# Performance work log

Hardware: AMD Instinct MI355X
Metric: run time of the kernel (lower is better)

Reference implementation:

```python
import jax, jax.numpy as jnp
import numpy as np

EPS = 1e-08

def _compute_W(V, C, eps=EPS):
    # W = H_k ... H_1, applied sequentially as in the torch loop
    W = jnp.eye(C, dtype=V.dtype)
    def step(W, v):
        v = v / (jnp.linalg.norm(v) + eps)
        # H @ W = W - 2 v (v^T W)
        W = W - 2.0 * jnp.outer(v, v @ W)
        return W, None
    W, _ = jax.lax.scan(step, W, V)
    return W

def setup_inputs() -> dict:
    key = jax.random.key(0)
    k1, k2 = jax.random.split(key)
    x = jax.random.normal(k1, (16, 512, 64, 64), dtype=jnp.float32)
    V = jax.random.normal(k2, (32, 512), dtype=jnp.float32)
    return {"x": x, "V": V}

def reference(x, V):
    B, C, H, Wd = x.shape
    W = _compute_W(V, C)  # [C, C] orthogonal
    # 1x1 conv: out[b,o,h,w] = sum_c W[o,c] * x[b,c,h,w]
    return jnp.einsum('oc,bchw->bohw', W, x)
```

## Files before the change

### kernel.cpp

```cpp
#include <hip/hip_runtime.h>
#include <hip/hip_bf16.h>
#include <stdint.h>
#include <stddef.h>

#define HH_EPS 1e-8f

typedef __attribute__((ext_vector_type(8))) short short8;
typedef __attribute__((ext_vector_type(4))) short short4_t;
typedef __attribute__((ext_vector_type(4))) float f32x4;

#define CDIM 512
#define SDIM 4096
#define BN 128
#define BK 32
#define NSTEP 16

__device__ __forceinline__ size_t wt_idx(int o, int c) {
    return (((size_t)(c >> 5) * 32 + (o >> 4)) * 64
            + (size_t)((c >> 3) & 3) * 16 + (o & 15)) * 8 + (c & 7);
}

__global__ void compute_w(const float* __restrict__ V,
                          __hip_bfloat16* __restrict__ Wt) {
    const int wave = threadIdx.x >> 6;
    const int lane = threadIdx.x & 63;
    const int jA = (blockIdx.x * 4 + wave) * 2;
    const int jB = jA + 1;
    const int ib = lane * 8;

    float wA[8], wB[8];
    #pragma unroll
    for (int r = 0; r < 8; r++) {
        wA[r] = (ib + r == jA) ? 1.0f : 0.0f;
        wB[r] = (ib + r == jB) ? 1.0f : 0.0f;
    }
    float4 c0 = *(const float4*)(V + ib);
    float4 c1 = *(const float4*)(V + ib + 4);

    for (int k = 0; k < 32; k++) {
        const float v[8] = {c0.x, c0.y, c0.z, c0.w, c1.x, c1.y, c1.z, c1.w};
        if (k < 31) {
            c0 = *(const float4*)(V + (size_t)(k + 1) * 512 + ib);
            c1 = *(const float4*)(V + (size_t)(k + 1) * 512 + ib + 4);
        }
        float dA = 0.0f, dB = 0.0f, ss = 0.0f;
        #pragma unroll
        for (int r = 0; r < 8; r++) {
            dA += v[r] * wA[r];
            dB += v[r] * wB[r];
            ss += v[r] * v[r];
        }
        #pragma unroll
        for (int off = 32; off > 0; off >>= 1) {
            dA += __shfl_xor(dA, off);
            dB += __shfl_xor(dB, off);
            ss += __shfl_xor(ss, off);
        }
        const float t = sqrtf(ss) + HH_EPS;
        const float scale = 2.0f / (t * t);
        const float tA = scale * dA, tB = scale * dB;
        #pragma unroll
        for (int r = 0; r < 8; r++) {
            wA[r] -= tA * v[r];
            wB[r] -= tB * v[r];
        }
    }
    #pragma unroll
    for (int r = 0; r < 8; r++) {
        Wt[wt_idx(ib + r, jA)] = __float2bfloat16(wA[r]);
        Wt[wt_idx(ib + r, jB)] = __float2bfloat16(wB[r]);
    }
}

__device__ __forceinline__ void lds_barrier() {
    __builtin_amdgcn_s_waitcnt(0xC07F);
    __builtin_amdgcn_s_barrier();
}

__global__ __launch_bounds__(1024, 4) void hh_gemm(
    const float* __restrict__ x,
    const __hip_bfloat16* __restrict__ Wt,
    float* __restrict__ out)
{
    __shared__ __attribute__((aligned(16))) __hip_bfloat16 Bbuf[2][BN * BK];

    const int tid  = threadIdx.x;
    const int wave = tid >> 6, lane = tid & 63;
    const int quad = lane >> 4, l16 = lane & 15;

    const int bid = blockIdx.x;
    const int b   = bid >> 5;
    const int nt  = bid & 31;
    const int n0  = nt * BN;

    const int c_s  = tid & 127;
    const int r0_s = (tid >> 7) * 4;
    const int kq_s = tid >> 8;
    const int h_s  = (tid >> 7) & 1;
    const float* xp0 = x + (size_t)b * CDIM * SDIM
                         + (size_t)r0_s * SDIM + n0 + c_s;

    const short8* wp = (const short8*)Wt + (size_t)(wave * 2) * 64 + lane;

    f32x4 acc[8][2];
    #pragma unroll
    for (int mi = 0; mi < 8; mi++)
        #pragma unroll
        for (int oi = 0; oi < 2; oi++) {
            f32x4 z = {0.0f, 0.0f, 0.0f, 0.0f};
            acc[mi][oi] = z;
        }

    float  pfB[2][4];
    short8 wb[2][2];

    auto loadB = [&](int kt, int s) {
        const float* p = xp0 + (size_t)kt * BK * SDIM;
        #pragma unroll
        for (int j = 0; j < 4; j++) pfB[s][j] = p[(size_t)j * SDIM];
    };
    auto writeB = [&](int buf, int s) {
        short4_t pk;
        #pragma unroll
        for (int j = 0; j < 4; j++) {
            __hip_bfloat16 h = __float2bfloat16(pfB[s][j]);
            pk[j] = *(const short*)&h;
        }
        *(short4_t*)(&Bbuf[buf][(size_t)(c_s >> 4) * 512
                                + (size_t)(kq_s * 16 + (c_s & 15)) * 8
                                + h_s * 4]) = pk;
    };
    auto loadW = [&](int kt, int s) {
        const short8* p = wp + (size_t)kt * 32 * 64;
        wb[s][0] = p[0];
        wb[s][1] = p[64];
    };

    loadB(0, 0);
    loadB(1, 1);
    loadW(0, 0);
    writeB(0, 0);
    lds_barrier();

    #pragma unroll
    for (int kt = 0; kt < NSTEP; kt++) {
        const int p = kt & 1, w = kt & 1;
        if (kt + 1 < NSTEP) loadW(kt + 1, w ^ 1);
        if (kt + 2 < NSTEP) loadB(kt + 2, kt & 1);
        #pragma unroll
        for (int mi = 0; mi < 8; mi++) {
            const short8 afr =
                *(const short8*)(&Bbuf[p][(size_t)(mi * 64 + lane) * 8]);
            #pragma unroll
            for (int oi = 0; oi < 2; oi++)
                acc[mi][oi] = __builtin_amdgcn_mfma_f32_16x16x32_bf16(
                    afr, wb[w][oi], acc[mi][oi], 0, 0, 0);
        }
        if (kt + 1 < NSTEP) {
            writeB(p ^ 1, (kt + 1) & 1);
            lds_barrier();
        }
    }

    float* ob = out + (size_t)b * CDIM * SDIM + n0;
    #pragma unroll
    for (int oi = 0; oi < 2; oi++) {
        const int o = wave * 32 + oi * 16 + l16;
        #pragma unroll
        for (int mi = 0; mi < 8; mi++)
            *(f32x4*)(ob + (size_t)o * SDIM + mi * 16 + quad * 4) = acc[mi][oi];
    }
}

extern "C" void kernel_launch(void* const* d_in, const int* in_sizes, int n_in,
                              void* d_out, int out_size, void* d_ws, size_t ws_size,
                              hipStream_t stream) {
    const float* x = (const float*)d_in[0];
    const float* V = (const float*)d_in[1];
    float* out = (float*)d_out;

    __hip_bfloat16* Wt = (__hip_bfloat16*)d_ws;

    compute_w<<<64, 256, 0, stream>>>(V, Wt);
    hh_gemm<<<512, 1024, 0, stream>>>(x, Wt, out);
}
```

Measured before the change: 265.6 us.

## Double K tile to 64 and load W fragments inline without prefetch

Raises the K tile from 32 to 64 channels, which halves the number of pipeline steps and LDS barriers. Each thread now loads 8 rows of x and writes one 16-byte bf16 vector to LDS instead of 8 bytes. The register double-buffer of W fragments is dropped, and W is loaded from global/L2 right before each half-step's MFMAs. This exposes W load latency and doubles the LDS buffer size to 32KB.

```diff
diff --git a/kernel.cpp b/kernel.cpp
--- a/kernel.cpp
+++ b/kernel.cpp
@@ -6,14 +6,13 @@
 #define HH_EPS 1e-8f
 
 typedef __attribute__((ext_vector_type(8))) short short8;
-typedef __attribute__((ext_vector_type(4))) short short4_t;
 typedef __attribute__((ext_vector_type(4))) float f32x4;
 
 #define CDIM 512
 #define SDIM 4096
 #define BN 128
-#define BK 32
-#define NSTEP 16
+#define BK 64
+#define NSTEP 8
 
 __device__ __forceinline__ size_t wt_idx(int o, int c) {
     return (((size_t)(c >> 5) * 32 + (o >> 4)) * 64
@@ -93,12 +92,12 @@
     const int nt  = bid & 31;
     const int n0  = nt * BN;
 
-    const int c_s  = tid & 127;
-    const int r0_s = (tid >> 7) * 4;
-    const int kq_s = tid >> 8;
-    const int h_s  = (tid >> 7) & 1;
+    const int c_s = tid & 127;
+    const int o8  = tid >> 7;
     const float* xp0 = x + (size_t)b * CDIM * SDIM
-                         + (size_t)r0_s * SDIM + n0 + c_s;
+                         + (size_t)(o8 * 8) * SDIM + n0 + c_s;
+    const size_t wslot = ((size_t)((o8 >> 2) * 8 + (c_s >> 4)) * 64
+                          + (size_t)((o8 & 3) * 16 + (c_s & 15))) * 8;
 
     const short8* wp = (const short8*)Wt + (size_t)(wave * 2) * 64 + lane;
 
@@ -111,50 +110,47 @@
             acc[mi][oi] = z;
         }
 
-    float  pfB[2][4];
-    short8 wb[2][2];
+    float pfB[2][8];
 
     auto loadB = [&](int kt, int s) {
         const float* p = xp0 + (size_t)kt * BK * SDIM;
         #pragma unroll
-        for (int j = 0; j < 4; j++) pfB[s][j] = p[(size_t)j * SDIM];
+        for (int j = 0; j < 8; j++) pfB[s][j] = p[(size_t)j * SDIM];
     };
     auto writeB = [&](int buf, int s) {
-        short4_t pk;
+        short8 pk;
         #pragma unroll
-        for (int j = 0; j < 4; j++) {
+        for (int j = 0; j < 8; j++) {
             __hip_bfloat16 h = __float2bfloat16(pfB[s][j]);
             pk[j] = *(const short*)&h;
         }
-        *(short4_t*)(&Bbuf[buf][(size_t)(c_s >> 4) * 512
-                                + (size_t)(kq_s * 16 + (c_s & 15)) * 8
-                                + h_s * 4]) = pk;
-    };
-    auto loadW = [&](int kt, int s) {
-        const short8* p = wp + (size_t)kt * 32 * 64;
-        wb[s][0] = p[0];
-        wb[s][1] = p[64];
+        *(short8*)(&Bbuf[buf][wslot]) = pk;
     };
 
     loadB(0, 0);
     loadB(1, 1);
-    loadW(0, 0);
     writeB(0, 0);
     lds_barrier();
 
     #pragma unroll
     for (int kt = 0; kt < NSTEP; kt++) {
-        const int p = kt & 1, w = kt & 1;
-        if (kt + 1 < NSTEP) loadW(kt + 1, w ^ 1);
+        const int p = kt & 1;
         if (kt + 2 < NSTEP) loadB(kt + 2, kt & 1);
         #pragma unroll
-        for (int mi = 0; mi < 8; mi++) {
-            const short8 afr =
-                *(const short8*)(&Bbuf[p][(size_t)(mi * 64 + lane) * 8]);
+        for (int kk = 0; kk < 2; kk++) {
+            short8 wf[2];
+            const short8* wq = wp + ((size_t)(kt * 2 + kk) * 32) * 64;
+            wf[0] = wq[0];
+            wf[1] = wq[64];
             #pragma unroll
-            for (int oi = 0; oi < 2; oi++)
-                acc[mi][oi] = __builtin_amdgcn_mfma_f32_16x16x32_bf16(
-                    afr, wb[w][oi], acc[mi][oi], 0, 0, 0);
+            for (int mi = 0; mi < 8; mi++) {
+                const short8 afr = *(const short8*)(
+                    &Bbuf[p][(size_t)((kk * 8 + mi) * 64 + lane) * 8]);
+                acc[mi][0] = __builtin_amdgcn_mfma_f32_16x16x32_bf16(
+                    afr, wf[0], acc[mi][0], 0, 0, 0);
+                acc[mi][1] = __builtin_amdgcn_mfma_f32_16x16x32_bf16(
+                    afr, wf[1], acc[mi][1], 0, 0, 0);
+            }
         }
         if (kt + 1 < NSTEP) {
             writeB(p ^ 1, (kt + 1) & 1);
```

Measured after the change: 264.7 us. No clear change (-0.4%).

## Vectorize x loads as float4, transpose via lane shuffles, deepen prefetch, remap blocks

Applied to the files above, without the earlier changes.

Each thread now loads x with a single float4 along the spatial dimension instead of four strided scalar loads down the channel dimension. The bf16 values are transposed into the MFMA operand layout with cross-lane shuffles before the LDS write. The x prefetch is deepened from two to three stages. Block indices are permuted so neighbouring blocks spread across batches, which may change cache and XCD locality. This aims to cut the number of global load instructions and improve coalescing, at the cost of extra shuffle and ALU work per step and more registers.

```diff
diff --git a/kernel.cpp b/kernel.cpp
--- a/kernel.cpp
+++ b/kernel.cpp
@@ -6,8 +6,8 @@
 #define HH_EPS 1e-8f
 
 typedef __attribute__((ext_vector_type(8))) short short8;
-typedef __attribute__((ext_vector_type(4))) short short4_t;
 typedef __attribute__((ext_vector_type(4))) float f32x4;
+typedef __attribute__((ext_vector_type(2))) unsigned int uint2_t;
 
 #define CDIM 512
 #define SDIM 4096
@@ -77,6 +77,11 @@
     __builtin_amdgcn_s_barrier();
 }
 
+__device__ __forceinline__ unsigned int bf16u(float f) {
+    __hip_bfloat16 h = __float2bfloat16(f);
+    return (unsigned int)*(unsigned short*)&h;
+}
+
 __global__ __launch_bounds__(1024, 4) void hh_gemm(
     const float* __restrict__ x,
     const __hip_bfloat16* __restrict__ Wt,
@@ -88,17 +93,21 @@
     const int wave = tid >> 6, lane = tid & 63;
     const int quad = lane >> 4, l16 = lane & 15;
 
-    const int bid = blockIdx.x;
+    const int bid = (blockIdx.x & 7) * 64 + (blockIdx.x >> 3);
     const int b   = bid >> 5;
     const int nt  = bid & 31;
     const int n0  = nt * BN;
 
-    const int c_s  = tid & 127;
-    const int r0_s = (tid >> 7) * 4;
-    const int kq_s = tid >> 8;
-    const int h_s  = (tid >> 7) & 1;
+    const int r_t    = lane >> 4;
+    const int kbase  = (wave & 7) * 4;
+    const int k_loc  = kbase + r_t;
+    const int n_loc  = (wave >> 3) * 64 + l16 * 4;
     const float* xp0 = x + (size_t)b * CDIM * SDIM
-                         + (size_t)r0_s * SDIM + n0 + c_s;
+                         + (size_t)k_loc * SDIM + n0 + n_loc;
+    const int n_tr   = (wave >> 3) * 64 + l16 * 4 + r_t;
+    const size_t wslot = ((size_t)(n_tr >> 4) * 64
+                          + (size_t)((wave & 7) >> 1) * 16 + (n_tr & 15)) * 8
+                         + (size_t)(wave & 1) * 4;
 
     const short8* wp = (const short8*)Wt + (size_t)(wave * 2) * 64 + lane;
 
@@ -111,33 +120,42 @@
             acc[mi][oi] = z;
         }
 
-    float  pfB[2][4];
+    float4 pfX[3];
     short8 wb[2][2];
 
-    auto loadB = [&](int kt, int s) {
-        const float* p = xp0 + (size_t)kt * BK * SDIM;
-        #pragma unroll
-        for (int j = 0; j < 4; j++) pfB[s][j] = p[(size_t)j * SDIM];
-    };
-    auto writeB = [&](int buf, int s) {
-        short4_t pk;
-        #pragma unroll
-        for (int j = 0; j < 4; j++) {
-            __hip_bfloat16 h = __float2bfloat16(pfB[s][j]);
-            pk[j] = *(const short*)&h;
-        }
-        *(short4_t*)(&Bbuf[buf][(size_t)(c_s >> 4) * 512
-                                + (size_t)(kq_s * 16 + (c_s & 15)) * 8
-                                + h_s * 4]) = pk;
+    auto loadX = [&](int kt, int s) {
+        pfX[s] = *(const float4*)(xp0 + (size_t)kt * BK * SDIM);
     };
     auto loadW = [&](int kt, int s) {
         const short8* p = wp + (size_t)kt * 32 * 64;
         wb[s][0] = p[0];
         wb[s][1] = p[64];
     };
-
-    loadB(0, 0);
-    loadB(1, 1);
+    auto writeB = [&](int buf, int s) {
+        const float4 v = pfX[s];
+        unsigned int A = bf16u(v.x) | (bf16u(v.y) << 16);
+        unsigned int B = bf16u(v.z) | (bf16u(v.w) << 16);
+        const unsigned int A1 = __shfl_xor((int)A, 16);
+        const unsigned int B1 = __shfl_xor((int)B, 16);
+        unsigned int pA, pB;
+        if ((r_t & 1) == 0) {
+            pA = (A & 0xffffu) | (A1 << 16);
+            pB = (B & 0xffffu) | (B1 << 16);
+        } else {
+            pA = (A1 >> 16) | (A & 0xffff0000u);
+            pB = (B1 >> 16) | (B & 0xffff0000u);
+        }
+        const unsigned int pA2 = __shfl_xor((int)pA, 32);
+        const unsigned int pB2 = __shfl_xor((int)pB, 32);
+        uint2_t w2;
+        if (r_t < 2) { w2[0] = pA;  w2[1] = pA2; }
+        else         { w2[0] = pB2; w2[1] = pB;  }
+        *(uint2_t*)(&Bbuf[buf][wslot]) = w2;
+    };
+
+    loadX(0, 0);
+    loadX(1, 1);
+    loadX(2, 2);
     loadW(0, 0);
     writeB(0, 0);
     lds_barrier();
@@ -146,18 +164,18 @@
     for (int kt = 0; kt < NSTEP; kt++) {
         const int p = kt & 1, w = kt & 1;
         if (kt + 1 < NSTEP) loadW(kt + 1, w ^ 1);
-        if (kt + 2 < NSTEP) loadB(kt + 2, kt & 1);
+        if (kt + 3 < NSTEP) loadX(kt + 3, kt % 3);
         #pragma unroll
         for (int mi = 0; mi < 8; mi++) {
             const short8 afr =
                 *(const short8*)(&Bbuf[p][(size_t)(mi * 64 + lane) * 8]);
-            #pragma unroll
-            for (int oi = 0; oi < 2; oi++)
-                acc[mi][oi] = __builtin_amdgcn_mfma_f32_16x16x32_bf16(
-                    afr, wb[w][oi], acc[mi][oi], 0, 0, 0);
+            acc[mi][0] = __builtin_amdgcn_mfma_f32_16x16x32_bf16(
+                afr, wb[w][0], acc[mi][0], 0, 0, 0);
+            acc[mi][1] = __builtin_amdgcn_mfma_f32_16x16x32_bf16(
+                afr, wb[w][1], acc[mi][1], 0, 0, 0);
         }
         if (kt + 1 < NSTEP) {
-            writeB(p ^ 1, (kt + 1) & 1);
+            writeB(p ^ 1, (kt + 1) % 3);
             lds_barrier();
         }
     }
```

Result: no change. 266.6 us (+0.4%).

## Split GEMM k-step into four barrier-separated phases interleaving loads with MFMA

Applied to the files above, without the earlier changes.

Each k-step of the bf16 MFMA GEMM is broken into four phases. Each phase issues two LDS fragment reads and one slice of the prefetch work (W load, x load, bf16 pack, LDS write), then runs four MFMAs at raised wave priority, with workgroup barriers around each phase. The aim is a ping-pong style schedule where memory issue and matrix work across the 16 waves stay in lockstep and overlap. The cost is eight barriers per k-step instead of one, which in a 1024-thread block may add stall time, and the waitcnt placement after the barrier may not strictly order the LDS write ahead of readers of the next buffer.

```diff
diff --git a/kernel.cpp b/kernel.cpp
--- a/kernel.cpp
+++ b/kernel.cpp
@@ -99,6 +99,8 @@
     const int h_s  = (tid >> 7) & 1;
     const float* xp0 = x + (size_t)b * CDIM * SDIM
                          + (size_t)r0_s * SDIM + n0 + c_s;
+    const size_t wslot = (size_t)(c_s >> 4) * 512
+                       + (size_t)(kq_s * 16 + (c_s & 15)) * 8 + h_s * 4;
 
     const short8* wp = (const short8*)Wt + (size_t)(wave * 2) * 64 + lane;
 
@@ -111,24 +113,24 @@
             acc[mi][oi] = z;
         }
 
-    float  pfB[2][4];
-    short8 wb[2][2];
+    float    pfB[2][4];
+    short8   wb[2][2];
+    short4_t pk;
 
     auto loadB = [&](int kt, int s) {
         const float* p = xp0 + (size_t)kt * BK * SDIM;
         #pragma unroll
         for (int j = 0; j < 4; j++) pfB[s][j] = p[(size_t)j * SDIM];
     };
-    auto writeB = [&](int buf, int s) {
-        short4_t pk;
+    auto packB = [&](int s) {
         #pragma unroll
         for (int j = 0; j < 4; j++) {
             __hip_bfloat16 h = __float2bfloat16(pfB[s][j]);
             pk[j] = *(const short*)&h;
         }
-        *(short4_t*)(&Bbuf[buf][(size_t)(c_s >> 4) * 512
-                                + (size_t)(kq_s * 16 + (c_s & 15)) * 8
-                                + h_s * 4]) = pk;
+    };
+    auto writePK = [&](int buf) {
+        *(short4_t*)(&Bbuf[buf][wslot]) = pk;
     };
     auto loadW = [&](int kt, int s) {
         const short8* p = wp + (size_t)kt * 32 * 64;
@@ -136,31 +138,55 @@
         wb[s][1] = p[64];
     };
 
+#define MFMA1(A, MI, OI)                                                       \
+    acc[MI][OI] = __builtin_amdgcn_mfma_f32_16x16x32_bf16(                     \
+        A, wb[P_][OI], acc[MI][OI], 0, 0, 0);
+
+#define PHASE(P_, Q, STAGE)                                                    \
+    {                                                                          \
+        const short8 a0 = *(const short8*)(                                    \
+            &Bbuf[P_][(size_t)(((Q) * 2 + 0) * 64 + lane) * 8]);               \
+        const short8 a1 = *(const short8*)(                                    \
+            &Bbuf[P_][(size_t)(((Q) * 2 + 1) * 64 + lane) * 8]);               \
+        STAGE;                                                                 \
+        __builtin_amdgcn_s_barrier();                                          \
+        __builtin_amdgcn_s_waitcnt(0xC07F);      \
+        __builtin_amdgcn_s_setprio(1);                                         \
+        acc[(Q)*2+0][0] = __builtin_amdgcn_mfma_f32_16x16x32_bf16(             \
+            a0, wb[P_][0], acc[(Q)*2+0][0], 0, 0, 0);                          \
+        acc[(Q)*2+0][1] = __builtin_amdgcn_mfma_f32_16x16x32_bf16(             \
+            a0, wb[P_][1], acc[(Q)*2+0][1], 0, 0, 0);                          \
+        acc[(Q)*2+1][0] = __builtin_amdgcn_mfma_f32_16x16x32_bf16(             \
+            a1, wb[P_][0], acc[(Q)*2+1][0], 0, 0, 0);                          \
+        acc[(Q)*2+1][1] = __builtin_amdgcn_mfma_f32_16x16x32_bf16(             \
+            a1, wb[P_][1], acc[(Q)*2+1][1], 0, 0, 0);                          \
+        __builtin_amdgcn_s_setprio(0);                                         \
+        __builtin_amdgcn_s_barrier();                                          \
+    }
+
     loadB(0, 0);
     loadB(1, 1);
     loadW(0, 0);
-    writeB(0, 0);
+    packB(0);
+    writePK(0);
     lds_barrier();
 
-    #pragma unroll
-    for (int kt = 0; kt < NSTEP; kt++) {
-        const int p = kt & 1, w = kt & 1;
-        if (kt + 1 < NSTEP) loadW(kt + 1, w ^ 1);
-        if (kt + 2 < NSTEP) loadB(kt + 2, kt & 1);
-        #pragma unroll
-        for (int mi = 0; mi < 8; mi++) {
-            const short8 afr =
-                *(const short8*)(&Bbuf[p][(size_t)(mi * 64 + lane) * 8]);
-            #pragma unroll
-            for (int oi = 0; oi < 2; oi++)
-                acc[mi][oi] = __builtin_amdgcn_mfma_f32_16x16x32_bf16(
-                    afr, wb[w][oi], acc[mi][oi], 0, 0, 0);
-        }
-        if (kt + 1 < NSTEP) {
-            writeB(p ^ 1, (kt + 1) & 1);
-            lds_barrier();
-        }
-    }
+#define DO_STEP(KT)                                                            \
+    {                                                                          \
+        constexpr int p = (KT) & 1;                                            \
+        PHASE(p, 0, if constexpr ((KT) + 1 < NSTEP) loadW((KT) + 1, p ^ 1))    \
+        PHASE(p, 1, if constexpr ((KT) + 2 < NSTEP) loadB((KT) + 2, (KT) & 1)) \
+        PHASE(p, 2, if constexpr ((KT) + 1 < NSTEP) packB(((KT) + 1) & 1))     \
+        PHASE(p, 3, if constexpr ((KT) + 1 < NSTEP) writePK(p ^ 1))            \
+    }
+
+    DO_STEP(0)  DO_STEP(1)  DO_STEP(2)  DO_STEP(3)
+    DO_STEP(4)  DO_STEP(5)  DO_STEP(6)  DO_STEP(7)
+    DO_STEP(8)  DO_STEP(9)  DO_STEP(10) DO_STEP(11)
+    DO_STEP(12) DO_STEP(13) DO_STEP(14) DO_STEP(15)
+#undef DO_STEP
+#undef PHASE
+#undef MFMA1
 
     float* ob = out + (size_t)b * CDIM * SDIM + n0;
     #pragma unroll
```

Measured after the change: 259.4 us. 2.4% less time.
